# Kernel optimization log

Measured on AMD Instinct MI355X. Metric: run time of the kernel, lower is better.

The kernel has to match this reference:

```python
import jax, jax.numpy as jnp
import numpy as np

H, B, D, C = 6, 512, 2048, 1000   # heads (5 ICs + backbone exit), batch, feat dim, classes
TAU = 0.5                          # confidence_threshold


def setup_inputs() -> dict:
    key = jax.random.key(0)
    k1, k2, k3, k4 = jax.random.split(key, 4)
    feats = jax.random.normal(k1, (H, B, D), dtype=jnp.float32)          # pooled reps at each exit
    W = jax.random.normal(k2, (H, D, C), dtype=jnp.float32) * 0.07       # per-head classifier weights
    b = jax.random.normal(k3, (H, C), dtype=jnp.float32) * 0.1
    y_true = jax.random.randint(k4, (B,), 0, C)
    return {"feats": feats, "W": W, "b": b, "y_true": y_true}


def reference(feats, W, b, y_true):
    # Per-head logits for every sample (vectorized replacement for the shrinking-batch loop).
    logits = jnp.einsum('hbd,hdc->hbc', feats, W) + b[:, None, :]        # [H, B, C]
    logp = jax.nn.log_softmax(logits, axis=-1)
    conf = jnp.exp(logp).max(axis=-1)                                    # [H, B] max softmax prob (prob_conf=True)

    # Early-exit routing: first head with conf >= TAU; else head with max confidence
    # (argmax returns the first occurrence, matching the strict '>' update in find_exit).
    exited = conf >= TAU                                                  # [H, B]
    any_exit = exited.any(axis=0)                                         # [B]
    first_exit = jnp.argmax(exited, axis=0)                               # [B] first True along heads
    best_conf = jnp.argmax(conf, axis=0)                                  # [B] fallback exit
    exit_idx = jnp.where(any_exit, first_exit, best_conf)                 # [B] == sample_exited_at

    # Gather the chosen head's logits per sample (vectorized masked-scatter of sample_outputs).
    outputs = jnp.take_along_axis(logits, exit_idx[None, :, None], axis=0)[0]   # [B, C]

    # criterion_ic: cross-entropy loss + accuracy on routed outputs
    out_logp = jax.nn.log_softmax(outputs, axis=-1)
    loss = -jnp.take_along_axis(out_logp, y_true[:, None], axis=1).mean()
    acc = (outputs.argmax(axis=-1) == y_true).astype(jnp.float32).mean()
    return outputs, exit_idx.astype(jnp.int32), loss, acc
```

## Files before the change

### kernel.cpp

```cpp
#include <hip/hip_runtime.h>
#include <math.h>

#define Hn 6
#define Bn 512
#define Dn 2048
#define Cn 1000
#define Cpad 1024
#define TAUv 0.5f
#define KSPLIT 4
#define KPER (Dn / KSPLIT)
#define KT 32
#define NIT (KPER / KT)
#define NKT (Dn / KT)

typedef unsigned int u32;
typedef unsigned short u16;
typedef __attribute__((ext_vector_type(8))) short short8;
typedef __attribute__((ext_vector_type(4))) float f32x4;

union FragU { u32 d[4]; short8 s; };

__device__ __forceinline__ u32 bf16_rne(float f) {
  const u32 u = __float_as_uint(f);
  return (u + 0x7FFFu + ((u >> 16) & 1u)) >> 16;
}
__device__ __forceinline__ u32 pack_rne2(float f0, float f1, float& r0, float& r1) {
  const u32 b0 = bf16_rne(f0), b1 = bf16_rne(f1);
  r0 = f0 - __uint_as_float(b0 << 16);
  r1 = f1 - __uint_as_float(b1 << 16);
  return b0 | (b1 << 16);
}

__device__ __forceinline__ void dma16(const void* g, void* l) {
  __builtin_amdgcn_global_load_lds(
      (const __attribute__((address_space(1))) u32*)g,
      (__attribute__((address_space(3))) u32*)l, 16, 0, 0);
}

__device__ __forceinline__ void pack8(const float* rr, uint4& hv, uint4& lv) {
  float x0, x1, x2, x3, y0, y1, y2, y3, d;
  hv.x = pack_rne2(rr[0], rr[1], x0, x1);
  hv.y = pack_rne2(rr[2], rr[3], x2, x3);
  hv.z = pack_rne2(rr[4], rr[5], y0, y1);
  hv.w = pack_rne2(rr[6], rr[7], y2, y3);
  lv.x = pack_rne2(x0, x1, d, d);
  lv.y = pack_rne2(x2, x3, d, d);
  lv.z = pack_rne2(y0, y1, d, d);
  lv.w = pack_rne2(y2, y3, d, d);
}

__global__ __launch_bounds__(256) void conv_k(
    const float* __restrict__ feats, const float* __restrict__ W,
    u16* __restrict__ Ah, u16* __restrict__ Al,
    u16* __restrict__ Bh, u16* __restrict__ Bl,
    float* __restrict__ scalars)
{
  __shared__ float smem[128 * 33];
  const int t   = blockIdx.x;
  const int yy  = blockIdx.y;
  const int h   = blockIdx.z;
  const int tid = threadIdx.x;

  if (t == 0 && yy == 0 && h == 0 && tid == 0) { scalars[0] = 0.f; scalars[1] = 0.f; }

  if (yy < 4) {
    const int r0 = yy * 128;
#pragma unroll
    for (int i = 0; i < 4; ++i) {
      const int f = i * 256 + tid;
      const int r = f >> 3, q = f & 7;
      const float4 v = *(const float4*)(feats + ((size_t)(h * Bn + r0 + r) * Dn + t * 32 + q * 4));
      smem[r * 33 + q * 4 + 0] = v.x; smem[r * 33 + q * 4 + 1] = v.y;
      smem[r * 33 + q * 4 + 2] = v.z; smem[r * 33 + q * 4 + 3] = v.w;
    }
    __syncthreads();
#pragma unroll
    for (int i = 0; i < 2; ++i) {
      const int j = i * 256 + tid;
      const int c = j >> 7, r = j & 127;
      float rr[8];
#pragma unroll
      for (int e = 0; e < 8; ++e) rr[e] = smem[r * 33 + c * 8 + e];
      uint4 hv, lv;
      pack8(rr, hv, lv);
      const size_t o = (((size_t)(h * 64 + t) * 4 + c) * 512 + r0 + r);
      ((uint4*)Ah)[o] = hv;
      ((uint4*)Al)[o] = lv;
    }
  } else {
    const int n0 = (yy - 4) * 128;
#pragma unroll
    for (int i = 0; i < 4; ++i) {
      const int f = i * 256 + tid;
      const int k = f >> 5, q = f & 31;
      const int n = n0 + q * 4;
      const float* src = W + ((size_t)h * Dn + t * 32 + k) * Cn;
      float4 v = make_float4(0.f, 0.f, 0.f, 0.f);
      if (n + 3 < Cn) {
        v = *(const float4*)(src + n);
      } else {
        if (n + 0 < Cn) v.x = src[n + 0];
        if (n + 1 < Cn) v.y = src[n + 1];
        if (n + 2 < Cn) v.z = src[n + 2];
        if (n + 3 < Cn) v.w = src[n + 3];
      }
      smem[k * 129 + q * 4 + 0] = v.x; smem[k * 129 + q * 4 + 1] = v.y;
      smem[k * 129 + q * 4 + 2] = v.z; smem[k * 129 + q * 4 + 3] = v.w;
    }
    __syncthreads();
#pragma unroll
    for (int i = 0; i < 2; ++i) {
      const int j = i * 256 + tid;
      const int c = j >> 7, n = j & 127;
      float rr[8];
#pragma unroll
      for (int e = 0; e < 8; ++e) rr[e] = smem[(c * 8 + e) * 129 + n];
      uint4 hv, lv;
      pack8(rr, hv, lv);
      const size_t o = (((size_t)(h * 64 + t) * 4 + c) * 1024 + n0 + n);
      ((uint4*)Bh)[o] = hv;
      ((uint4*)Bl)[o] = lv;
    }
  }
}

__global__ __launch_bounds__(256, 3) void gemm_k(
    const u16* __restrict__ AhG, const u16* __restrict__ AlG,
    const u16* __restrict__ BhG, const u16* __restrict__ BlG,
    const float* __restrict__ bias, float* __restrict__ logits)
{
  const int h  = blockIdx.z >> 2;
  const int kz = blockIdx.z & 3;
  const int m0 = blockIdx.y * 128;
  const int n0 = blockIdx.x * 128;

  __shared__ __align__(16) short Ah[4][128][8];
  __shared__ __align__(16) short Al[4][128][8];
  __shared__ __align__(16) short Bh[4][128][8];
  __shared__ __align__(16) short Bl[4][128][8];

  const int t = threadIdx.x;
  const int lane = t & 63;
  const int w    = t >> 6;
  const int wm   = (w & 1) * 64;
  const int wn   = (w >> 1) * 64;
  const int fl   = lane & 15;
  const int fq   = lane >> 4;

  const u16* gmat = (w == 0) ? AhG : (w == 1) ? AlG : (w == 2) ? BhG : BlG;
  const int  R    = (w < 2) ? 512 : 1024;
  const int  row0 = (w < 2) ? m0 : n0;
  short* lbase = (w == 0) ? &Ah[0][0][0] : (w == 1) ? &Al[0][0][0]
               : (w == 2) ? &Bh[0][0][0] : &Bl[0][0][0];
  const uint4* g0 = (const uint4*)gmat
                  + ((size_t)(h * 64 + kz * NIT) * 4) * R + row0 + lane;

  f32x4 acc[4][4];
#pragma unroll
  for (int i = 0; i < 4; ++i)
#pragma unroll
    for (int j = 0; j < 4; ++j) acc[i][j] = (f32x4){0.f, 0.f, 0.f, 0.f};

  for (int it = 0; it < NIT; ++it) {
    const size_t ito = (size_t)(it * 4) * R;
#pragma unroll
    for (int c = 0; c < 4; ++c) {
      dma16(g0 + ito + (size_t)c * R,      lbase + (c * 128) * 8);
      dma16(g0 + ito + (size_t)c * R + 64, lbase + (c * 128 + 64) * 8);
    }
    __syncthreads();

    FragU ah[4], al[4];
#pragma unroll
    for (int mt = 0; mt < 4; ++mt) {
      const int m = wm + mt * 16 + fl;
      ah[mt].s = *(const short8*)(&Ah[fq][m][0]);
      al[mt].s = *(const short8*)(&Al[fq][m][0]);
    }
#pragma unroll
    for (int nt = 0; nt < 4; ++nt) {
      const int n = wn + nt * 16 + fl;
      FragU bh, bl;
      bh.s = *(const short8*)(&Bh[fq][n][0]);
      bl.s = *(const short8*)(&Bl[fq][n][0]);
#pragma unroll
      for (int mt = 0; mt < 4; ++mt) {
        acc[mt][nt] = __builtin_amdgcn_mfma_f32_16x16x32_bf16(ah[mt].s, bh.s, acc[mt][nt], 0, 0, 0);
        acc[mt][nt] = __builtin_amdgcn_mfma_f32_16x16x32_bf16(ah[mt].s, bl.s, acc[mt][nt], 0, 0, 0);
        acc[mt][nt] = __builtin_amdgcn_mfma_f32_16x16x32_bf16(al[mt].s, bh.s, acc[mt][nt], 0, 0, 0);
      }
    }
    __syncthreads();
  }

  float* part = logits + (size_t)kz * ((size_t)Hn * Bn * Cn);
#pragma unroll
  for (int nt = 0; nt < 4; ++nt) {
    const int col = n0 + wn + nt * 16 + fl;
    if (col >= Cn) continue;
    const float bv = (kz == 0) ? bias[(size_t)h * Cn + col] : 0.f;
#pragma unroll
    for (int mt = 0; mt < 4; ++mt) {
      const int rbase = m0 + wm + mt * 16 + fq * 4;
#pragma unroll
      for (int r = 0; r < 4; ++r)
        part[((size_t)h * Bn + rbase + r) * Cn + col] = acc[mt][nt][r] + bv;
    }
  }
}

__global__ __launch_bounds__(256) void confpick_k(
    const float* __restrict__ logits, const int* __restrict__ y,
    float* __restrict__ out, float* __restrict__ out_exit,
    float* __restrict__ scalars)
{
  const int b = blockIdx.x, tid = threadIdx.x;
  const int lane = tid & 63, w = tid >> 6;
  const size_t S = (size_t)Hn * Bn * Cn;
  __shared__ float ms[Hn], ss[Hn];

  for (int h = w; h < Hn; h += 4) {
    const float* p = logits + ((size_t)h * Bn + b) * Cn;
    float vv[16];
#pragma unroll
    for (int i = 0; i < 4; ++i) {
      const int c4 = i * 256 + lane * 4;
      if (c4 + 3 < Cn) {
        const float4 v0 = *(const float4*)(p + c4);
        const float4 v1 = *(const float4*)(p + S + c4);
        const float4 v2 = *(const float4*)(p + 2 * S + c4);
        const float4 v3 = *(const float4*)(p + 3 * S + c4);
        vv[4 * i + 0] = v0.x + v1.x + v2.x + v3.x;
        vv[4 * i + 1] = v0.y + v1.y + v2.y + v3.y;
        vv[4 * i + 2] = v0.z + v1.z + v2.z + v3.z;
        vv[4 * i + 3] = v0.w + v1.w + v2.w + v3.w;
      } else {
#pragma unroll
        for (int j = 0; j < 4; ++j) {
          const int c = c4 + j;
          vv[4 * i + j] = (c < Cn) ? p[c] + p[S + c] + p[2 * S + c] + p[3 * S + c]
                                   : -3.4e38f;
        }
      }
    }
    float m = -3.4e38f;
#pragma unroll
    for (int i = 0; i < 16; ++i) m = fmaxf(m, vv[i]);
#pragma unroll
    for (int off = 32; off >= 1; off >>= 1) m = fmaxf(m, __shfl_xor(m, off));
    float s = 0.f;
#pragma unroll
    for (int i = 0; i < 16; ++i) s += (vv[i] > -3.0e38f) ? expf(vv[i] - m) : 0.f;
#pragma unroll
    for (int off = 32; off >= 1; off >>= 1) s += __shfl_xor(s, off);
    if (lane == 0) { ms[h] = m; ss[h] = s; }
  }
  __syncthreads();

  int first = -1, best = 0;
  float bestc = -3.4e38f;
#pragma unroll
  for (int h = 0; h < Hn; ++h) {
    const float c = 1.0f / ss[h];
    if (first < 0 && c >= TAUv) first = h;
    if (c > bestc) { bestc = c; best = h; }
  }
  const int ex = (first >= 0) ? first : best;
  const float* p = logits + ((size_t)ex * Bn + b) * Cn;

  const int c4 = tid * 4;
  float vv[4] = {-3.4e38f, -3.4e38f, -3.4e38f, -3.4e38f};
  if (c4 + 3 < Cn) {
    const float4 v0 = *(const float4*)(p + c4);
    const float4 v1 = *(const float4*)(p + S + c4);
    const float4 v2 = *(const float4*)(p + 2 * S + c4);
    const float4 v3 = *(const float4*)(p + 3 * S + c4);
    vv[0] = v0.x + v1.x + v2.x + v3.x;
    vv[1] = v0.y + v1.y + v2.y + v3.y;
    vv[2] = v0.z + v1.z + v2.z + v3.z;
    vv[3] = v0.w + v1.w + v2.w + v3.w;
  }
  float vm = -3.4e38f; int im = 1 << 30;
#pragma unroll
  for (int j = 0; j < 4; ++j) {
    const int c = c4 + j;
    if (c < Cn) {
      out[(size_t)b * Cn + c] = vv[j];
      if (vv[j] > vm) { vm = vv[j]; im = c; }
    }
  }
#pragma unroll
  for (int off = 32; off >= 1; off >>= 1) {
    const float ov = __shfl_xor(vm, off);
    const int   oi = __shfl_xor(im, off);
    if (ov > vm || (ov == vm && oi < im)) { vm = ov; im = oi; }
  }
  __shared__ float rm[4]; __shared__ int ri[4];
  if (lane == 0) { rm[w] = vm; ri[w] = im; }
  __syncthreads();
  if (tid == 0) {
    float bm = rm[0]; int bi = ri[0];
    for (int q = 1; q < 4; ++q)
      if (rm[q] > bm || (rm[q] == bm && ri[q] < bi)) { bm = rm[q]; bi = ri[q]; }
    const int yt = y[b];
    const float ryt = p[yt] + p[S + yt] + p[2 * S + yt] + p[3 * S + yt];
    const float lp = ryt - ms[ex] - logf(ss[ex]);
    out_exit[b] = (float)ex;
    atomicAdd(&scalars[0], -lp * (1.0f / (float)Bn));
    atomicAdd(&scalars[1], ((bi == yt) ? 1.f : 0.f) * (1.0f / (float)Bn));
  }
}

extern "C" void kernel_launch(void* const* d_in, const int* in_sizes, int n_in,
                              void* d_out, int out_size, void* d_ws, size_t ws_size,
                              hipStream_t stream) {
  const float* feats = (const float*)d_in[0];
  const float* W     = (const float*)d_in[1];
  const float* bias  = (const float*)d_in[2];
  const int*   y     = (const int*)d_in[3];
  float* out = (float*)d_out;

  float* logits = (float*)d_ws;
  u16*   AhG    = (u16*)(logits + (size_t)KSPLIT * Hn * Bn * Cn);
  u16*   AlG    = AhG + (size_t)Hn * Bn * Dn;
  u16*   BhG    = AlG + (size_t)Hn * Bn * Dn;
  u16*   BlG    = BhG + (size_t)Hn * Cpad * Dn;

  float* out_exit    = out + (size_t)Bn * Cn;
  float* out_scalars = out + (size_t)Bn * Cn + Bn;

  conv_k<<<dim3(NKT, 12, Hn), 256, 0, stream>>>(feats, W, AhG, AlG, BhG, BlG, out_scalars);
  gemm_k<<<dim3(Cpad / 128, Bn / 128, Hn * KSPLIT), 256, 0, stream>>>(
      AhG, AlG, BhG, BlG, bias, logits);
  confpick_k<<<Bn, 256, 0, stream>>>(logits, y, out, out_exit, out_scalars);
}
```

Measured before the change: 189.0 us.

## Fuse bf16 split conversion into GEMM with fp32 LDS double buffering

Removes the separate conversion kernel that wrote hi/lo bf16 copies of feats and W to workspace. The GEMM now DMAs raw fp32 tiles into a double-buffered, XOR-swizzled LDS region and converts to hi/lo bf16 fragments in registers just before the MFMAs. Occupancy drops to 2 blocks per CU. This saves a kernel launch and the global write and read-back of the converted operands. In exchange every block repeats the conversion work, reads twice as many bytes per tile (fp32 instead of bf16), and uses more LDS, with strided scalar LDS reads for B.

```diff
diff --git a/kernel.cpp b/kernel.cpp
--- a/kernel.cpp
+++ b/kernel.cpp
@@ -1,4 +1,5 @@
 #include <hip/hip_runtime.h>
+#include <hip/hip_bf16.h>
 #include <math.h>
 
 #define Hn 6
@@ -9,9 +10,7 @@
 #define TAUv 0.5f
 #define KSPLIT 4
 #define KPER (Dn / KSPLIT)
-#define KT 32
-#define NIT (KPER / KT)
-#define NKT (Dn / KT)
+#define NIT (KPER / 32)
 
 typedef unsigned int u32;
 typedef unsigned short u16;
@@ -20,15 +19,23 @@
 
 union FragU { u32 d[4]; short8 s; };
 
-__device__ __forceinline__ u32 bf16_rne(float f) {
-  const u32 u = __float_as_uint(f);
-  return (u + 0x7FFFu + ((u >> 16) & 1u)) >> 16;
-}
-__device__ __forceinline__ u32 pack_rne2(float f0, float f1, float& r0, float& r1) {
-  const u32 b0 = bf16_rne(f0), b1 = bf16_rne(f1);
-  r0 = f0 - __uint_as_float(b0 << 16);
-  r1 = f1 - __uint_as_float(b1 << 16);
-  return b0 | (b1 << 16);
+__device__ __forceinline__ u32 cvt_pk2(float f0, float f1) {
+  union { __hip_bfloat162 h; u32 u; } cv;
+  cv.h = __float22bfloat162_rn(make_float2(f0, f1));
+  return cv.u;
+}
+
+__device__ __forceinline__ void pack8f(const float* f, FragU& hi, FragU& lo) {
+  float r[8];
+#pragma unroll
+  for (int i = 0; i < 4; ++i) {
+    const u32 d = cvt_pk2(f[2 * i], f[2 * i + 1]);
+    hi.d[i] = d;
+    r[2 * i]     = f[2 * i]     - __uint_as_float(d << 16);
+    r[2 * i + 1] = f[2 * i + 1] - __uint_as_float(d & 0xffff0000u);
+  }
+#pragma unroll
+  for (int i = 0; i < 4; ++i) lo.d[i] = cvt_pk2(r[2 * i], r[2 * i + 1]);
 }
 
 __device__ __forceinline__ void dma16(const void* g, void* l) {
@@ -37,123 +44,44 @@
       (__attribute__((address_space(3))) u32*)l, 16, 0, 0);
 }
 
-__device__ __forceinline__ void pack8(const float* rr, uint4& hv, uint4& lv) {
-  float x0, x1, x2, x3, y0, y1, y2, y3, d;
-  hv.x = pack_rne2(rr[0], rr[1], x0, x1);
-  hv.y = pack_rne2(rr[2], rr[3], x2, x3);
-  hv.z = pack_rne2(rr[4], rr[5], y0, y1);
-  hv.w = pack_rne2(rr[6], rr[7], y2, y3);
-  lv.x = pack_rne2(x0, x1, d, d);
-  lv.y = pack_rne2(x2, x3, d, d);
-  lv.z = pack_rne2(y0, y1, d, d);
-  lv.w = pack_rne2(y2, y3, d, d);
-}
-
-__global__ __launch_bounds__(256) void conv_k(
+__global__ __launch_bounds__(256, 2) void gemm_k(
     const float* __restrict__ feats, const float* __restrict__ W,
-    u16* __restrict__ Ah, u16* __restrict__ Al,
-    u16* __restrict__ Bh, u16* __restrict__ Bl,
+    const float* __restrict__ bias, float* __restrict__ logits,
     float* __restrict__ scalars)
-{
-  __shared__ float smem[128 * 33];
-  const int t   = blockIdx.x;
-  const int yy  = blockIdx.y;
-  const int h   = blockIdx.z;
-  const int tid = threadIdx.x;
-
-  if (t == 0 && yy == 0 && h == 0 && tid == 0) { scalars[0] = 0.f; scalars[1] = 0.f; }
-
-  if (yy < 4) {
-    const int r0 = yy * 128;
-#pragma unroll
-    for (int i = 0; i < 4; ++i) {
-      const int f = i * 256 + tid;
-      const int r = f >> 3, q = f & 7;
-      const float4 v = *(const float4*)(feats + ((size_t)(h * Bn + r0 + r) * Dn + t * 32 + q * 4));
-      smem[r * 33 + q * 4 + 0] = v.x; smem[r * 33 + q * 4 + 1] = v.y;
-      smem[r * 33 + q * 4 + 2] = v.z; smem[r * 33 + q * 4 + 3] = v.w;
-    }
-    __syncthreads();
-#pragma unroll
-    for (int i = 0; i < 2; ++i) {
-      const int j = i * 256 + tid;
-      const int c = j >> 7, r = j & 127;
-      float rr[8];
-#pragma unroll
-      for (int e = 0; e < 8; ++e) rr[e] = smem[r * 33 + c * 8 + e];
-      uint4 hv, lv;
-      pack8(rr, hv, lv);
-      const size_t o = (((size_t)(h * 64 + t) * 4 + c) * 512 + r0 + r);
-      ((uint4*)Ah)[o] = hv;
-      ((uint4*)Al)[o] = lv;
-    }
-  } else {
-    const int n0 = (yy - 4) * 128;
-#pragma unroll
-    for (int i = 0; i < 4; ++i) {
-      const int f = i * 256 + tid;
-      const int k = f >> 5, q = f & 31;
-      const int n = n0 + q * 4;
-      const float* src = W + ((size_t)h * Dn + t * 32 + k) * Cn;
-      float4 v = make_float4(0.f, 0.f, 0.f, 0.f);
-      if (n + 3 < Cn) {
-        v = *(const float4*)(src + n);
-      } else {
-        if (n + 0 < Cn) v.x = src[n + 0];
-        if (n + 1 < Cn) v.y = src[n + 1];
-        if (n + 2 < Cn) v.z = src[n + 2];
-        if (n + 3 < Cn) v.w = src[n + 3];
-      }
-      smem[k * 129 + q * 4 + 0] = v.x; smem[k * 129 + q * 4 + 1] = v.y;
-      smem[k * 129 + q * 4 + 2] = v.z; smem[k * 129 + q * 4 + 3] = v.w;
-    }
-    __syncthreads();
-#pragma unroll
-    for (int i = 0; i < 2; ++i) {
-      const int j = i * 256 + tid;
-      const int c = j >> 7, n = j & 127;
-      float rr[8];
-#pragma unroll
-      for (int e = 0; e < 8; ++e) rr[e] = smem[(c * 8 + e) * 129 + n];
-      uint4 hv, lv;
-      pack8(rr, hv, lv);
-      const size_t o = (((size_t)(h * 64 + t) * 4 + c) * 1024 + n0 + n);
-      ((uint4*)Bh)[o] = hv;
-      ((uint4*)Bl)[o] = lv;
-    }
-  }
-}
-
-__global__ __launch_bounds__(256, 3) void gemm_k(
-    const u16* __restrict__ AhG, const u16* __restrict__ AlG,
-    const u16* __restrict__ BhG, const u16* __restrict__ BlG,
-    const float* __restrict__ bias, float* __restrict__ logits)
 {
   const int h  = blockIdx.z >> 2;
   const int kz = blockIdx.z & 3;
   const int m0 = blockIdx.y * 128;
   const int n0 = blockIdx.x * 128;
-
-  __shared__ __align__(16) short Ah[4][128][8];
-  __shared__ __align__(16) short Al[4][128][8];
-  __shared__ __align__(16) short Bh[4][128][8];
-  __shared__ __align__(16) short Bl[4][128][8];
-
-  const int t = threadIdx.x;
-  const int lane = t & 63;
-  const int w    = t >> 6;
-  const int wm   = (w & 1) * 64;
-  const int wn   = (w >> 1) * 64;
-  const int fl   = lane & 15;
-  const int fq   = lane >> 4;
-
-  const u16* gmat = (w == 0) ? AhG : (w == 1) ? AlG : (w == 2) ? BhG : BlG;
-  const int  R    = (w < 2) ? 512 : 1024;
-  const int  row0 = (w < 2) ? m0 : n0;
-  short* lbase = (w == 0) ? &Ah[0][0][0] : (w == 1) ? &Al[0][0][0]
-               : (w == 2) ? &Bh[0][0][0] : &Bl[0][0][0];
-  const uint4* g0 = (const uint4*)gmat
-                  + ((size_t)(h * 64 + kz * NIT) * 4) * R + row0 + lane;
+  const int t = threadIdx.x, lane = t & 63, w = t >> 6;
+
+  if (t == 0 && blockIdx.x == 0 && blockIdx.y == 0 && blockIdx.z == 0) {
+    scalars[0] = 0.f; scalars[1] = 0.f;
+  }
+
+  __shared__ __align__(16) float lds[2][8192];
+
+  const float* gsrc; size_t gci, gadv; int dst0;
+  if (w < 2) {
+    const int r = w * 64 + (lane >> 3);
+    const int q = (lane & 7) ^ ((lane >> 3) & 7);
+    gsrc = feats + ((size_t)(h * Bn + m0 + r)) * Dn + kz * KPER + q * 4;
+    gci  = (size_t)8 * Dn;
+    gadv = 32;
+    dst0 = w * 8192 + lane * 16;
+  } else {
+    const int kk  = (w - 2) * 16 + (lane >> 5);
+    const int c4  = n0 + (lane & 31) * 4;
+    const int c4c = (c4 + 3 < Cn) ? c4 : (Cn - 4);
+    gsrc = W + ((size_t)h * Dn + kz * KPER + kk) * Cn + c4c;
+    gci  = (size_t)2 * Cn;
+    gadv = (size_t)32 * Cn;
+    dst0 = 16384 + (w - 2) * 8192 + lane * 16;
+  }
+
+  const int fl = lane & 15, fq = lane >> 4;
+  const int wm = (w & 1) * 64, wn = (w >> 1) * 64;
+  const int sxor = fl & 7;
 
   f32x4 acc[4][4];
 #pragma unroll
@@ -161,37 +89,53 @@
 #pragma unroll
     for (int j = 0; j < 4; ++j) acc[i][j] = (f32x4){0.f, 0.f, 0.f, 0.f};
 
-  for (int it = 0; it < NIT; ++it) {
-    const size_t ito = (size_t)(it * 4) * R;
-#pragma unroll
-    for (int c = 0; c < 4; ++c) {
-      dma16(g0 + ito + (size_t)c * R,      lbase + (c * 128) * 8);
-      dma16(g0 + ito + (size_t)c * R + 64, lbase + (c * 128 + 64) * 8);
-    }
+  {
+    char* sb = (char*)&lds[0][0];
+#pragma unroll
+    for (int i = 0; i < 8; ++i) dma16(gsrc + i * gci, sb + dst0 + i * 1024);
+  }
+  __syncthreads();
+
+#define COMPUTE_TILE(IT)                                                              \
+  {                                                                                   \
+    const char*  ab = (const char*)&lds[(IT) & 1][0];                                 \
+    const float* bb = (const float*)(ab + 16384);                                     \
+    FragU ah[4], al[4];                                                               \
+    _Pragma("unroll")                                                                 \
+    for (int mt = 0; mt < 4; ++mt) {                                                  \
+      const int r = wm + mt * 16 + fl;                                                \
+      const float4 v0 = *(const float4*)(ab + r * 128 + ((((fq * 2)    ) ^ sxor) * 16)); \
+      const float4 v1 = *(const float4*)(ab + r * 128 + ((((fq * 2) + 1) ^ sxor) * 16)); \
+      float f[8] = {v0.x, v0.y, v0.z, v0.w, v1.x, v1.y, v1.z, v1.w};                  \
+      pack8f(f, ah[mt], al[mt]);                                                      \
+    }                                                                                 \
+    _Pragma("unroll")                                                                 \
+    for (int nt = 0; nt < 4; ++nt) {                                                  \
+      const int n = wn + nt * 16 + fl;                                                \
+      float f[8];                                                                     \
+      _Pragma("unroll")                                                               \
+      for (int e = 0; e < 8; ++e) f[e] = bb[(fq * 8 + e) * 128 + n];                  \
+      FragU bh, bl;                                                                   \
+      pack8f(f, bh, bl);                                                              \
+      _Pragma("unroll")                                                               \
+      for (int mt = 0; mt < 4; ++mt) {                                                \
+        acc[mt][nt] = __builtin_amdgcn_mfma_f32_16x16x32_bf16(ah[mt].s, bh.s, acc[mt][nt], 0, 0, 0); \
+        acc[mt][nt] = __builtin_amdgcn_mfma_f32_16x16x32_bf16(ah[mt].s, bl.s, acc[mt][nt], 0, 0, 0); \
+        acc[mt][nt] = __builtin_amdgcn_mfma_f32_16x16x32_bf16(al[mt].s, bh.s, acc[mt][nt], 0, 0, 0); \
+      }                                                                               \
+    }                                                                                 \
+  }
+
+  for (int it = 0; it < NIT - 1; ++it) {
+    char* sb = (char*)&lds[(it + 1) & 1][0];
+    const float* g = gsrc + (size_t)(it + 1) * gadv;
+#pragma unroll
+    for (int i = 0; i < 8; ++i) dma16(g + i * gci, sb + dst0 + i * 1024);
+    COMPUTE_TILE(it);
     __syncthreads();
-
-    FragU ah[4], al[4];
-#pragma unroll
-    for (int mt = 0; mt < 4; ++mt) {
-      const int m = wm + mt * 16 + fl;
-      ah[mt].s = *(const short8*)(&Ah[fq][m][0]);
-      al[mt].s = *(const short8*)(&Al[fq][m][0]);
-    }
-#pragma unroll
-    for (int nt = 0; nt < 4; ++nt) {
-      const int n = wn + nt * 16 + fl;
-      FragU bh, bl;
-      bh.s = *(const short8*)(&Bh[fq][n][0]);
-      bl.s = *(const short8*)(&Bl[fq][n][0]);
-#pragma unroll
-      for (int mt = 0; mt < 4; ++mt) {
-        acc[mt][nt] = __builtin_amdgcn_mfma_f32_16x16x32_bf16(ah[mt].s, bh.s, acc[mt][nt], 0, 0, 0);
-        acc[mt][nt] = __builtin_amdgcn_mfma_f32_16x16x32_bf16(ah[mt].s, bl.s, acc[mt][nt], 0, 0, 0);
-        acc[mt][nt] = __builtin_amdgcn_mfma_f32_16x16x32_bf16(al[mt].s, bh.s, acc[mt][nt], 0, 0, 0);
-      }
-    }
-    __syncthreads();
-  }
+  }
+  COMPUTE_TILE(NIT - 1);
+#undef COMPUTE_TILE
 
   float* part = logits + (size_t)kz * ((size_t)Hn * Bn * Cn);
 #pragma unroll
@@ -321,16 +265,10 @@
   float* out = (float*)d_out;
 
   float* logits = (float*)d_ws;
-  u16*   AhG    = (u16*)(logits + (size_t)KSPLIT * Hn * Bn * Cn);
-  u16*   AlG    = AhG + (size_t)Hn * Bn * Dn;
-  u16*   BhG    = AlG + (size_t)Hn * Bn * Dn;
-  u16*   BlG    = BhG + (size_t)Hn * Cpad * Dn;
-
   float* out_exit    = out + (size_t)Bn * Cn;
   float* out_scalars = out + (size_t)Bn * Cn + Bn;
 
-  conv_k<<<dim3(NKT, 12, Hn), 256, 0, stream>>>(feats, W, AhG, AlG, BhG, BlG, out_scalars);
   gemm_k<<<dim3(Cpad / 128, Bn / 128, Hn * KSPLIT), 256, 0, stream>>>(
-      AhG, AlG, BhG, BlG, bias, logits);
+      feats, W, bias, logits, out_scalars);
   confpick_k<<<Bn, 256, 0, stream>>>(logits, y, out, out_exit, out_scalars);
 }
```

Result: no change. 191.8 us (+1.5%).
